# Performance work log

Measured on AMD Instinct MI355X. Metric: run time of the kernel, lower is better.

The kernel has to match this reference:

```python
import jax, jax.numpy as jnp
import numpy as np

N = 50000      # nodes
K = 15         # k_max candidate neighbors per node
D = 128        # node_dim
H = 64         # hidden_dim
K_MIN = 2.0
K_MAX = 15.0
TAU = 0.5      # edge_tau
LAM = 1.0      # selector_lambda


def setup_inputs() -> dict:
    key = jax.random.key(0)
    ks = jax.random.split(key, 16)
    x = jax.random.normal(ks[0], (N, D), dtype=jnp.float32)
    src = jax.random.randint(ks[1], (N * K,), 0, N)
    dst = jnp.repeat(jnp.arange(N), K)  # edges grouped by dst, as the module requires
    edge_index = jnp.stack([src, dst]).astype(jnp.int64)
    edge_dist = jax.random.uniform(ks[2], (N * K,), dtype=jnp.float32)

    def lin(k, fin, fout):
        return jax.random.normal(k, (fin, fout), dtype=jnp.float32) / np.sqrt(fin)

    EIN = 2 * D + 1  # edge MLP input: [x_dst, x_src, dist]
    return {
        "x": x, "edge_index": edge_index, "edge_dist": edge_dist,
        "ew1": lin(ks[3], EIN, H), "eb1": jnp.zeros((H,), jnp.float32),
        "ew2": lin(ks[4], H, H),   "eb2": jnp.zeros((H,), jnp.float32),
        "ew3": lin(ks[5], H, 1),   "eb3": jnp.zeros((1,), jnp.float32),
        "dw1": lin(ks[6], D + 1, H), "db1": jnp.zeros((H,), jnp.float32),
        "dw2": lin(ks[7], H, H),     "db2": jnp.zeros((H,), jnp.float32),
        "dw3": lin(ks[8], H, 1),     "db3": jnp.zeros((1,), jnp.float32),
    }


def reference(x, edge_index, edge_dist, ew1, eb1, ew2, eb2, ew3, eb3,
              dw1, db1, dw2, db2, dw3, db3):
    src_mat = edge_index[0].reshape(N, K)              # (N, K)
    x_src = x[src_mat]                                 # gather: (N, K, D)
    x_dst = jnp.broadcast_to(x[:, None, :], (N, K, D))
    edge_feat = jnp.concatenate([x_dst, x_src, edge_dist.reshape(N, K, 1)], axis=-1)

    # edge MLP -> logits (eval mode: no gumbel-logistic noise)
    h = jax.nn.relu(edge_feat @ ew1 + eb1)
    h = jax.nn.relu(h @ ew2 + eb2)
    edge_logits = (h @ ew3 + eb3)[..., 0]              # (N, K)
    edge_energy = jax.nn.sigmoid(edge_logits / TAU)

    # degree MLP -> continuous k per node
    degree_hint = edge_energy.sum(axis=1, keepdims=True)
    g = jax.nn.relu(jnp.concatenate([x, degree_hint], axis=1) @ dw1 + db1)
    g = jax.nn.relu(g @ dw2 + db2)
    k_raw = (g @ dw3 + db3)[:, 0]
    k_cont = K_MIN + (K_MAX - K_MIN) * jax.nn.sigmoid(k_raw)  # (N,)

    # per-node descending sort + straight-through top-k gate
    perm = jnp.argsort(-edge_energy, axis=1)
    energy_sorted = jnp.take_along_axis(edge_energy, perm, axis=1)
    ranks = jnp.arange(1, K + 1, dtype=x.dtype)[None, :]
    gate_soft = jax.nn.sigmoid((k_cont[:, None] - ranks) / LAM)
    k_int = jnp.clip(jnp.round(k_cont), K_MIN, K_MAX)
    gate_hard = (ranks <= k_int[:, None]).astype(gate_soft.dtype)
    gate = gate_soft + jax.lax.stop_gradient(gate_hard - gate_soft)

    gated_sorted = energy_sorted * gate
    inv_perm = jnp.argsort(perm, axis=1)               # undo the sort
    edge_gate = jnp.take_along_axis(gate, inv_perm, axis=1)
    edge_weight = jnp.take_along_axis(gated_sorted, inv_perm, axis=1)

    denom = jnp.maximum(edge_weight.sum(axis=1, keepdims=True), 1e-12)
    edge_weight = edge_weight / denom
    return (edge_weight.reshape(-1), edge_gate.reshape(-1),
            edge_energy.reshape(-1), k_cont)
```

## Files before the change

kernel.cpp:

```cpp
#include <hip/hip_runtime.h>
#include <cmath>

#define NN 50000
#define KK 15
#define DD 128
#define HH 64
#define NKE (NN * KK)

__global__ __launch_bounds__(256, 4) void kP(const float* __restrict__ x,
                                             const float* __restrict__ ew1,
                                             const float* __restrict__ dw1,
                                             float* __restrict__ ws) {
    int lane = threadIdx.x & 63;
    int wv = threadIdx.x >> 6;
    int r0 = blockIdx.x * 32 + wv * 8;
    if (r0 >= NN) return;

    const float* W0 = ew1;
    const float* W1 = ew1 + DD * HH;
    const float* W2 = dw1;
    const float* xw = x + (size_t)r0 * DD;

    float a0[8], a1[8], a2[8];
#pragma unroll
    for (int r = 0; r < 8; ++r) { a0[r] = 0.f; a1[r] = 0.f; a2[r] = 0.f; }

#pragma unroll 1
    for (int i4 = 0; i4 < DD / 4; ++i4) {
        float w00 = W0[(i4 * 4 + 0) * HH + lane];
        float w01 = W0[(i4 * 4 + 1) * HH + lane];
        float w02 = W0[(i4 * 4 + 2) * HH + lane];
        float w03 = W0[(i4 * 4 + 3) * HH + lane];
        float w10 = W1[(i4 * 4 + 0) * HH + lane];
        float w11 = W1[(i4 * 4 + 1) * HH + lane];
        float w12 = W1[(i4 * 4 + 2) * HH + lane];
        float w13 = W1[(i4 * 4 + 3) * HH + lane];
        float w20 = W2[(i4 * 4 + 0) * HH + lane];
        float w21 = W2[(i4 * 4 + 1) * HH + lane];
        float w22 = W2[(i4 * 4 + 2) * HH + lane];
        float w23 = W2[(i4 * 4 + 3) * HH + lane];
#pragma unroll
        for (int r = 0; r < 8; ++r) {
            float4 xv = *(const float4*)(xw + r * DD + i4 * 4);
            a0[r] = fmaf(xv.x, w00, a0[r]);
            a0[r] = fmaf(xv.y, w01, a0[r]);
            a0[r] = fmaf(xv.z, w02, a0[r]);
            a0[r] = fmaf(xv.w, w03, a0[r]);
            a1[r] = fmaf(xv.x, w10, a1[r]);
            a1[r] = fmaf(xv.y, w11, a1[r]);
            a1[r] = fmaf(xv.z, w12, a1[r]);
            a1[r] = fmaf(xv.w, w13, a1[r]);
            a2[r] = fmaf(xv.x, w20, a2[r]);
            a2[r] = fmaf(xv.y, w21, a2[r]);
            a2[r] = fmaf(xv.z, w22, a2[r]);
            a2[r] = fmaf(xv.w, w23, a2[r]);
        }
    }
    float* o0 = ws + (size_t)r0 * HH + lane;
    float* o1 = ws + (size_t)NN * HH + (size_t)r0 * HH + lane;
    float* o2 = ws + 2 * (size_t)NN * HH + (size_t)r0 * HH + lane;
#pragma unroll
    for (int r = 0; r < 8; ++r) {
        o0[r * HH] = a0[r];
        o1[r * HH] = a1[r];
        o2[r * HH] = a2[r];
    }
}

__global__ __launch_bounds__(128, 4) void kE(const int* __restrict__ srcIdx,
                                             const float* __restrict__ dist,
                                             const float* __restrict__ ws,
                                             const float* __restrict__ ew1,
                                             const float* __restrict__ eb1,
                                             const float* __restrict__ ew2,
                                             const float* __restrict__ eb2,
                                             const float* __restrict__ ew3,
                                             const float* __restrict__ eb3,
                                             float* __restrict__ energy_out) {
    int e = blockIdx.x * 128 + threadIdx.x;
    if (e >= NKE) return;
    int s = srcIdx[e];
    int d = e / KK;
    float dd = dist[e];
    const float* A = ws + (size_t)d * HH;
    const float* B = ws + (size_t)NN * HH + (size_t)s * HH;
    const float* w1l = ew1 + 2 * DD * HH;

    float acc[HH];
#pragma unroll
    for (int j = 0; j < HH; ++j) acc[j] = 0.f;

    float4 a4 = *(const float4*)A;
    float4 bp0 = *(const float4*)B;
    float4 bp1 = *(const float4*)(B + 4);
#pragma unroll 1
    for (int i4 = 0; i4 < HH / 4; ++i4) {
        float4 a = a4, b = bp0;
        int n1 = (i4 + 1 < 16) ? (i4 + 1) : 15;
        int n2 = (i4 + 2 < 16) ? (i4 + 2) : 15;
        a4 = *(const float4*)(A + n1 * 4);
        bp0 = bp1;
        bp1 = *(const float4*)(B + n2 * 4);
        float h[4];
        h[0] = fmaxf(a.x + b.x + dd * w1l[i4 * 4 + 0] + eb1[i4 * 4 + 0], 0.f);
        h[1] = fmaxf(a.y + b.y + dd * w1l[i4 * 4 + 1] + eb1[i4 * 4 + 1], 0.f);
        h[2] = fmaxf(a.z + b.z + dd * w1l[i4 * 4 + 2] + eb1[i4 * 4 + 2], 0.f);
        h[3] = fmaxf(a.w + b.w + dd * w1l[i4 * 4 + 3] + eb1[i4 * 4 + 3], 0.f);
#pragma unroll
        for (int k = 0; k < 4; ++k) {
            const float* wr = ew2 + (i4 * 4 + k) * HH;
#pragma unroll
            for (int j4 = 0; j4 < 16; ++j4) {
                float4 w = *(const float4*)(wr + j4 * 4);
                acc[j4 * 4 + 0] = fmaf(h[k], w.x, acc[j4 * 4 + 0]);
                acc[j4 * 4 + 1] = fmaf(h[k], w.y, acc[j4 * 4 + 1]);
                acc[j4 * 4 + 2] = fmaf(h[k], w.z, acc[j4 * 4 + 2]);
                acc[j4 * 4 + 3] = fmaf(h[k], w.w, acc[j4 * 4 + 3]);
            }
        }
    }
    float lg = eb3[0];
#pragma unroll
    for (int j = 0; j < HH; ++j)
        lg = fmaf(fmaxf(acc[j] + eb2[j], 0.f), ew3[j], lg);
    energy_out[e] = 1.f / (1.f + expf(-2.f * lg));
}

__global__ __launch_bounds__(256, 4) void kF(const float* __restrict__ ws,
                                             const float* __restrict__ dw1,
                                             const float* __restrict__ db1,
                                             const float* __restrict__ dw2,
                                             const float* __restrict__ db2,
                                             const float* __restrict__ dw3,
                                             const float* __restrict__ db3,
                                             float* __restrict__ out) {
    int n = blockIdx.x * 256 + threadIdx.x;
    if (n >= NN) return;
    const float* energy = out + 2 * (size_t)NKE;

    float ev[KK];
    float dh = 0.f;
#pragma unroll
    for (int j = 0; j < KK; ++j) {
        ev[j] = energy[(size_t)n * KK + j];
        dh += ev[j];
    }

    const float* XC = ws + 2 * (size_t)NN * HH + (size_t)n * HH;
    const float* w1l = dw1 + DD * HH;
    float kraw = db3[0];

#pragma unroll 1
    for (int c = 0; c < 4; ++c) {
        float acc[16];
#pragma unroll
        for (int t = 0; t < 16; ++t) acc[t] = 0.f;
#pragma unroll 1
        for (int k4 = 0; k4 < 16; ++k4) {
            float4 cx = *(const float4*)(XC + k4 * 4);
            float cv[4] = {cx.x, cx.y, cx.z, cx.w};
#pragma unroll
            for (int m = 0; m < 4; ++m) {
                int k = k4 * 4 + m;
                float g = fmaxf(cv[m] + dh * w1l[k] + db1[k], 0.f);
                const float* wr = dw2 + k * HH + c * 16;
                float4 wA = *(const float4*)(wr + 0);
                float4 wB = *(const float4*)(wr + 4);
                float4 wC = *(const float4*)(wr + 8);
                float4 wD = *(const float4*)(wr + 12);
                acc[0]  = fmaf(g, wA.x, acc[0]);  acc[1]  = fmaf(g, wA.y, acc[1]);
                acc[2]  = fmaf(g, wA.z, acc[2]);  acc[3]  = fmaf(g, wA.w, acc[3]);
                acc[4]  = fmaf(g, wB.x, acc[4]);  acc[5]  = fmaf(g, wB.y, acc[5]);
                acc[6]  = fmaf(g, wB.z, acc[6]);  acc[7]  = fmaf(g, wB.w, acc[7]);
                acc[8]  = fmaf(g, wC.x, acc[8]);  acc[9]  = fmaf(g, wC.y, acc[9]);
                acc[10] = fmaf(g, wC.z, acc[10]); acc[11] = fmaf(g, wC.w, acc[11]);
                acc[12] = fmaf(g, wD.x, acc[12]); acc[13] = fmaf(g, wD.y, acc[13]);
                acc[14] = fmaf(g, wD.z, acc[14]); acc[15] = fmaf(g, wD.w, acc[15]);
            }
        }
#pragma unroll
        for (int t = 0; t < 16; ++t)
            kraw = fmaf(fmaxf(acc[t] + db2[c * 16 + t], 0.f), dw3[c * 16 + t], kraw);
    }

    float kcont = 2.f + 13.f / (1.f + expf(-kraw));
    out[3 * (size_t)NKE + n] = kcont;

    float se[16];
    int si[16];
#pragma unroll
    for (int j = 0; j < KK; ++j) { se[j] = ev[j]; si[j] = j; }
    se[15] = -1.f; si[15] = 15;

#pragma unroll
    for (int p = 1; p < 16; p <<= 1) {
#pragma unroll
        for (int k = p; k >= 1; k >>= 1) {
#pragma unroll
            for (int j = k & (p - 1); j + k < 16; j += 2 * k) {
#pragma unroll
                for (int i = 0; i < k; ++i) {
                    int a = i + j, b = i + j + k;
                    if (b < 16 && (a / (2 * p)) == (b / (2 * p))) {
                        bool sw = (se[b] > se[a]) ||
                                  (se[b] == se[a] && si[b] < si[a]);
                        float ea = sw ? se[b] : se[a];
                        float eb = sw ? se[a] : se[b];
                        int ia = sw ? si[b] : si[a];
                        int ib = sw ? si[a] : si[b];
                        se[a] = ea; se[b] = eb; si[a] = ia; si[b] = ib;
                    }
                }
            }
        }
    }

    float kint = rintf(kcont);
    kint = fminf(fmaxf(kint, 2.f), 15.f);

    float wsrt[KK];
    float denom = 0.f;
#pragma unroll
    for (int r = 0; r < KK; ++r) {
        float sel = ((float)(r + 1) <= kint) ? 1.f : 0.f;
        float wvv = se[r] * sel;
        wsrt[r] = wvv;
        denom += wvv;
    }
    denom = fmaxf(denom, 1e-12f);

#pragma unroll
    for (int r = 0; r < KK; ++r) {
        float sel = ((float)(r + 1) <= kint) ? 1.f : 0.f;
        int j0 = si[r];
        out[(size_t)NKE + (size_t)n * KK + j0] = sel;
        out[(size_t)n * KK + j0] = wsrt[r] / denom;
    }
}

extern "C" void kernel_launch(void* const* d_in, const int* in_sizes, int n_in,
                              void* d_out, int out_size, void* d_ws, size_t ws_size,
                              hipStream_t stream) {
    const float* x   = (const float*)d_in[0];
    const int*   ei  = (const int*)d_in[1];
    const float* ed  = (const float*)d_in[2];
    const float* ew1 = (const float*)d_in[3];
    const float* eb1 = (const float*)d_in[4];
    const float* ew2 = (const float*)d_in[5];
    const float* eb2 = (const float*)d_in[6];
    const float* ew3 = (const float*)d_in[7];
    const float* eb3 = (const float*)d_in[8];
    const float* dw1 = (const float*)d_in[9];
    const float* db1 = (const float*)d_in[10];
    const float* dw2 = (const float*)d_in[11];
    const float* db2 = (const float*)d_in[12];
    const float* dw3 = (const float*)d_in[13];
    const float* db3 = (const float*)d_in[14];
    float* out = (float*)d_out;
    float* ws  = (float*)d_ws;

    hipLaunchKernelGGL(kP, dim3((NN + 31) / 32), dim3(256), 0, stream,
                       x, ew1, dw1, ws);
    hipLaunchKernelGGL(kE, dim3((NKE + 127) / 128), dim3(128), 0, stream,
                       ei, ed, ws, ew1, eb1, ew2, eb2, ew3, eb3,
                       out + 2 * (size_t)NKE);
    hipLaunchKernelGGL(kF, dim3((NN + 255) / 256), dim3(256), 0, stream,
                       ws, dw1, db1, dw2, db2, dw3, db3, out);
}
```

Baseline: 316.8 us.

## Split degree MLP into wave-per-node kernel and use readlane broadcasts in projection

The degree MLP moves from one thread per node, where each thread loops over the full 64x64 weight matrix through memory, to one wavefront per node. Each lane keeps a column of dw2 in registers and receives broadcast values through readlane. The sort and gate part becomes a separate kernel that reads k_cont back from the output. The projection kernel also loads the x rows into registers once, coalesced, and broadcasts elements with readlane instead of issuing repeated float4 loads per row. Together these aim to cut redundant weight and memory traffic, at the cost of an extra kernel launch and serial readlane chains.

```diff
diff --git a/kernel.cpp b/kernel.cpp
--- a/kernel.cpp
+++ b/kernel.cpp
@@ -7,54 +7,64 @@
 #define HH 64
 #define NKE (NN * KK)
 
-__global__ __launch_bounds__(256, 4) void kP(const float* __restrict__ x,
-                                             const float* __restrict__ ew1,
-                                             const float* __restrict__ dw1,
-                                             float* __restrict__ ws) {
+#define RLF(v, l) __uint_as_float(__builtin_amdgcn_readlane(__float_as_uint(v), (l)))
+
+__global__ __launch_bounds__(256, 4) void kP3(const float* __restrict__ x,
+                                              const float* __restrict__ ew1,
+                                              const float* __restrict__ dw1,
+                                              float* __restrict__ ws) {
     int lane = threadIdx.x & 63;
     int wv = threadIdx.x >> 6;
     int r0 = blockIdx.x * 32 + wv * 8;
     if (r0 >= NN) return;
 
+    const float4* xg = (const float4*)(x + (size_t)r0 * DD);
+    float4 xs0 = xg[0 * 64 + lane];
+    float4 xs1 = xg[1 * 64 + lane];
+    float4 xs2 = xg[2 * 64 + lane];
+    float4 xs3 = xg[3 * 64 + lane];
+
     const float* W0 = ew1;
     const float* W1 = ew1 + DD * HH;
     const float* W2 = dw1;
-    const float* xw = x + (size_t)r0 * DD;
 
     float a0[8], a1[8], a2[8];
 #pragma unroll
     for (int r = 0; r < 8; ++r) { a0[r] = 0.f; a1[r] = 0.f; a2[r] = 0.f; }
 
 #pragma unroll 1
-    for (int i4 = 0; i4 < DD / 4; ++i4) {
-        float w00 = W0[(i4 * 4 + 0) * HH + lane];
-        float w01 = W0[(i4 * 4 + 1) * HH + lane];
-        float w02 = W0[(i4 * 4 + 2) * HH + lane];
-        float w03 = W0[(i4 * 4 + 3) * HH + lane];
-        float w10 = W1[(i4 * 4 + 0) * HH + lane];
-        float w11 = W1[(i4 * 4 + 1) * HH + lane];
-        float w12 = W1[(i4 * 4 + 2) * HH + lane];
-        float w13 = W1[(i4 * 4 + 3) * HH + lane];
-        float w20 = W2[(i4 * 4 + 0) * HH + lane];
-        float w21 = W2[(i4 * 4 + 1) * HH + lane];
-        float w22 = W2[(i4 * 4 + 2) * HH + lane];
-        float w23 = W2[(i4 * 4 + 3) * HH + lane];
-#pragma unroll
-        for (int r = 0; r < 8; ++r) {
-            float4 xv = *(const float4*)(xw + r * DD + i4 * 4);
-            a0[r] = fmaf(xv.x, w00, a0[r]);
-            a0[r] = fmaf(xv.y, w01, a0[r]);
-            a0[r] = fmaf(xv.z, w02, a0[r]);
-            a0[r] = fmaf(xv.w, w03, a0[r]);
-            a1[r] = fmaf(xv.x, w10, a1[r]);
-            a1[r] = fmaf(xv.y, w11, a1[r]);
-            a1[r] = fmaf(xv.z, w12, a1[r]);
-            a1[r] = fmaf(xv.w, w13, a1[r]);
-            a2[r] = fmaf(xv.x, w20, a2[r]);
-            a2[r] = fmaf(xv.y, w21, a2[r]);
-            a2[r] = fmaf(xv.z, w22, a2[r]);
-            a2[r] = fmaf(xv.w, w23, a2[r]);
+    for (int k4 = 0; k4 < DD / 4; ++k4) {
+        float w00 = W0[(k4 * 4 + 0) * HH + lane];
+        float w01 = W0[(k4 * 4 + 1) * HH + lane];
+        float w02 = W0[(k4 * 4 + 2) * HH + lane];
+        float w03 = W0[(k4 * 4 + 3) * HH + lane];
+        float w10 = W1[(k4 * 4 + 0) * HH + lane];
+        float w11 = W1[(k4 * 4 + 1) * HH + lane];
+        float w12 = W1[(k4 * 4 + 2) * HH + lane];
+        float w13 = W1[(k4 * 4 + 3) * HH + lane];
+        float w20 = W2[(k4 * 4 + 0) * HH + lane];
+        float w21 = W2[(k4 * 4 + 1) * HH + lane];
+        float w22 = W2[(k4 * 4 + 2) * HH + lane];
+        float w23 = W2[(k4 * 4 + 3) * HH + lane];
+        int lsE = k4;
+        int lsO = 32 + k4;
+
+#define KP_ROW(r, S, L)                                                    \
+        {                                                                  \
+            float xk0 = RLF(S.x, L), xk1 = RLF(S.y, L);                    \
+            float xk2 = RLF(S.z, L), xk3 = RLF(S.w, L);                    \
+            a0[r] = fmaf(xk0, w00, a0[r]); a0[r] = fmaf(xk1, w01, a0[r]);  \
+            a0[r] = fmaf(xk2, w02, a0[r]); a0[r] = fmaf(xk3, w03, a0[r]);  \
+            a1[r] = fmaf(xk0, w10, a1[r]); a1[r] = fmaf(xk1, w11, a1[r]);  \
+            a1[r] = fmaf(xk2, w12, a1[r]); a1[r] = fmaf(xk3, w13, a1[r]);  \
+            a2[r] = fmaf(xk0, w20, a2[r]); a2[r] = fmaf(xk1, w21, a2[r]);  \
+            a2[r] = fmaf(xk2, w22, a2[r]); a2[r] = fmaf(xk3, w23, a2[r]);  \
         }
+        KP_ROW(0, xs0, lsE) KP_ROW(1, xs0, lsO)
+        KP_ROW(2, xs1, lsE) KP_ROW(3, xs1, lsO)
+        KP_ROW(4, xs2, lsE) KP_ROW(5, xs2, lsO)
+        KP_ROW(6, xs3, lsE) KP_ROW(7, xs3, lsO)
+#undef KP_ROW
     }
     float* o0 = ws + (size_t)r0 * HH + lane;
     float* o1 = ws + (size_t)NN * HH + (size_t)r0 * HH + lane;
@@ -69,7 +79,7 @@
 
 __global__ __launch_bounds__(128, 4) void kE(const int* __restrict__ srcIdx,
                                              const float* __restrict__ dist,
-                                             const float* __restrict__ ws,
+                                             const float* __restrict__ xabc,
                                              const float* __restrict__ ew1,
                                              const float* __restrict__ eb1,
                                              const float* __restrict__ ew2,
@@ -82,8 +92,8 @@
     int s = srcIdx[e];
     int d = e / KK;
     float dd = dist[e];
-    const float* A = ws + (size_t)d * HH;
-    const float* B = ws + (size_t)NN * HH + (size_t)s * HH;
+    const float* A = xabc + (size_t)d * HH;
+    const float* B = xabc + (size_t)NN * HH + (size_t)s * HH;
     const float* w1l = ew1 + 2 * DD * HH;
 
     float acc[HH];
@@ -126,65 +136,61 @@
     energy_out[e] = 1.f / (1.f + expf(-2.f * lg));
 }
 
-__global__ __launch_bounds__(256, 4) void kF(const float* __restrict__ ws,
-                                             const float* __restrict__ dw1,
-                                             const float* __restrict__ db1,
-                                             const float* __restrict__ dw2,
-                                             const float* __restrict__ db2,
-                                             const float* __restrict__ dw3,
-                                             const float* __restrict__ db3,
-                                             float* __restrict__ out) {
+#define KF1_BLOCKS 782
+__global__ __launch_bounds__(256, 4) void kF1(const float* __restrict__ xabc,
+                                              const float* __restrict__ dw1,
+                                              const float* __restrict__ db1,
+                                              const float* __restrict__ dw2,
+                                              const float* __restrict__ db2,
+                                              const float* __restrict__ dw3,
+                                              const float* __restrict__ db3,
+                                              float* __restrict__ out) {
+    int lane = threadIdx.x & 63;
+    int wgid = blockIdx.x * 4 + (threadIdx.x >> 6);
+    const int nwaves = KF1_BLOCKS * 4;
+    const float* energy = out + 2 * (size_t)NKE;
+    const float* XC = xabc + 2 * (size_t)NN * HH;
+
+    float w2col[HH];
+#pragma unroll
+    for (int j = 0; j < HH; ++j) w2col[j] = dw2[j * HH + lane];
+    float w1l_l = dw1[DD * HH + lane];
+    float db1_l = db1[lane];
+    float db2_l = db2[lane];
+    float dw3_l = dw3[lane];
+    float db3s = db3[0];
+
+#pragma unroll 1
+    for (int n = wgid; n < NN; n += nwaves) {
+        float ev = 0.f;
+        if (lane < KK) ev = energy[(size_t)n * KK + lane];
+        float dh = 0.f;
+#pragma unroll
+        for (int j = 0; j < KK; ++j) dh += RLF(ev, j);
+        float g = fmaxf(XC[(size_t)n * HH + lane] + dh * w1l_l + db1_l, 0.f);
+        float acc = 0.f;
+#pragma unroll
+        for (int j = 0; j < HH; ++j)
+            acc = fmaf(RLF(g, j), w2col[j], acc);
+        float tv = fmaxf(acc + db2_l, 0.f);
+        float kraw = db3s;
+#pragma unroll
+        for (int t = 0; t < HH; ++t)
+            kraw = fmaf(RLF(tv, t), RLF(dw3_l, t), kraw);
+        float kcont = 2.f + 13.f / (1.f + expf(-kraw));
+        if (lane == 0) out[3 * (size_t)NKE + n] = kcont;
+    }
+}
+
+__global__ __launch_bounds__(256, 4) void kG(float* __restrict__ out) {
     int n = blockIdx.x * 256 + threadIdx.x;
     if (n >= NN) return;
     const float* energy = out + 2 * (size_t)NKE;
 
     float ev[KK];
-    float dh = 0.f;
-#pragma unroll
-    for (int j = 0; j < KK; ++j) {
-        ev[j] = energy[(size_t)n * KK + j];
-        dh += ev[j];
-    }
-
-    const float* XC = ws + 2 * (size_t)NN * HH + (size_t)n * HH;
-    const float* w1l = dw1 + DD * HH;
-    float kraw = db3[0];
-
-#pragma unroll 1
-    for (int c = 0; c < 4; ++c) {
-        float acc[16];
-#pragma unroll
-        for (int t = 0; t < 16; ++t) acc[t] = 0.f;
-#pragma unroll 1
-        for (int k4 = 0; k4 < 16; ++k4) {
-            float4 cx = *(const float4*)(XC + k4 * 4);
-            float cv[4] = {cx.x, cx.y, cx.z, cx.w};
-#pragma unroll
-            for (int m = 0; m < 4; ++m) {
-                int k = k4 * 4 + m;
-                float g = fmaxf(cv[m] + dh * w1l[k] + db1[k], 0.f);
-                const float* wr = dw2 + k * HH + c * 16;
-                float4 wA = *(const float4*)(wr + 0);
-                float4 wB = *(const float4*)(wr + 4);
-                float4 wC = *(const float4*)(wr + 8);
-                float4 wD = *(const float4*)(wr + 12);
-                acc[0]  = fmaf(g, wA.x, acc[0]);  acc[1]  = fmaf(g, wA.y, acc[1]);
-                acc[2]  = fmaf(g, wA.z, acc[2]);  acc[3]  = fmaf(g, wA.w, acc[3]);
-                acc[4]  = fmaf(g, wB.x, acc[4]);  acc[5]  = fmaf(g, wB.y, acc[5]);
-                acc[6]  = fmaf(g, wB.z, acc[6]);  acc[7]  = fmaf(g, wB.w, acc[7]);
-                acc[8]  = fmaf(g, wC.x, acc[8]);  acc[9]  = fmaf(g, wC.y, acc[9]);
-                acc[10] = fmaf(g, wC.z, acc[10]); acc[11] = fmaf(g, wC.w, acc[11]);
-                acc[12] = fmaf(g, wD.x, acc[12]); acc[13] = fmaf(g, wD.y, acc[13]);
-                acc[14] = fmaf(g, wD.z, acc[14]); acc[15] = fmaf(g, wD.w, acc[15]);
-            }
-        }
-#pragma unroll
-        for (int t = 0; t < 16; ++t)
-            kraw = fmaf(fmaxf(acc[t] + db2[c * 16 + t], 0.f), dw3[c * 16 + t], kraw);
-    }
-
-    float kcont = 2.f + 13.f / (1.f + expf(-kraw));
-    out[3 * (size_t)NKE + n] = kcont;
+#pragma unroll
+    for (int j = 0; j < KK; ++j) ev[j] = energy[(size_t)n * KK + j];
+    float kcont = out[3 * (size_t)NKE + n];
 
     float se[16];
     int si[16];
@@ -259,11 +265,12 @@
     float* out = (float*)d_out;
     float* ws  = (float*)d_ws;
 
-    hipLaunchKernelGGL(kP, dim3((NN + 31) / 32), dim3(256), 0, stream,
+    hipLaunchKernelGGL(kP3, dim3((NN + 31) / 32), dim3(256), 0, stream,
                        x, ew1, dw1, ws);
     hipLaunchKernelGGL(kE, dim3((NKE + 127) / 128), dim3(128), 0, stream,
                        ei, ed, ws, ew1, eb1, ew2, eb2, ew3, eb3,
                        out + 2 * (size_t)NKE);
-    hipLaunchKernelGGL(kF, dim3((NN + 255) / 256), dim3(256), 0, stream,
+    hipLaunchKernelGGL(kF1, dim3(KF1_BLOCKS), dim3(256), 0, stream,
                        ws, dw1, db1, dw2, db2, dw3, db3, out);
-}
+    hipLaunchKernelGGL(kG, dim3((NN + 255) / 256), dim3(256), 0, stream, out);
+}
```

Measured after the change: 327.9 us. +3.5%, slower.
